# Kernel tuning notes

Measured on AMD Instinct MI355X. Metric: run time of the kernel, lower is better.

Reference implementation:

```python
import jax, jax.numpy as jnp
import numpy as np

B, T, D, HS = 8, 2048, 1024, 64  # batch, seq, num_embd, head_size


def setup_inputs() -> dict:
    key = jax.random.key(0)
    kc, kq, kk, kv = jax.random.split(key, 4)
    return {
        "context": jax.random.normal(kc, (B, T, D), dtype=jnp.float32),
        "Wq": jax.random.normal(kq, (D, HS), dtype=jnp.float32) * (D ** -0.5),
        "Wk": jax.random.normal(kk, (D, HS), dtype=jnp.float32) * (D ** -0.5),
        "Wv": jax.random.normal(kv, (D, HS), dtype=jnp.float32) * (D ** -0.5),
    }


def reference(context, Wq, Wk, Wv):
    # context: [B, T, D]; projections: [B, T, HS]
    q = context @ Wq
    k = context @ Wk
    v = context @ Wv
    scale = k.shape[-1] ** -0.5
    # scores: [B, T, T], causal mask, stable softmax (dropout p=0 -> identity)
    wei = jnp.einsum("btd,bsd->bts", q, k) * scale
    t = wei.shape[-1]
    causal = jnp.tril(jnp.ones((t, t), dtype=bool))
    wei = jnp.where(causal, wei, -jnp.inf)
    wei = jax.nn.softmax(wei, axis=-1)
    return jnp.einsum("bts,bsh->bth", wei, v)
```

## Files before the change

kernel.cpp:

```cpp
#include <hip/hip_runtime.h>
#include <math.h>

#define BB 8
#define TT 2048
#define DD 1024
#define HSZ 64

typedef __bf16 bf16_t;
typedef bf16_t bf16x8 __attribute__((ext_vector_type(8)));
typedef bf16_t bf16x4 __attribute__((ext_vector_type(4)));
typedef float f32x4 __attribute__((ext_vector_type(4)));

#define MFMA16(A, B, C) __builtin_amdgcn_mfma_f32_16x16x32_bf16(A, B, C, 0, 0, 0)


__global__ __launch_bounds__(256) void wt_convert(
    const float* __restrict__ Wq, const float* __restrict__ Wk,
    const float* __restrict__ Wv, bf16_t* __restrict__ Wtf)
{
    int id = blockIdx.x * 256 + threadIdx.x;
    int j = id & 7;
    int lane = (id >> 3) & 63;
    int chunk = (id >> 9) & 31;
    int nt = id >> 14;
    int l16 = lane & 15, quad = lane >> 4;
    int k = chunk * 32 + quad * 8 + j;
    int col = nt * 16 + l16;
    int m = col >> 6, ncol = col & 63;
    const float* W = (m == 0) ? Wq : (m == 1) ? Wk : Wv;
    float scl = (m == 0) ? 0.18033688f : 1.0f;
    Wtf[id] = (bf16_t)(W[k * HSZ + ncol] * scl);
}

__global__ __launch_bounds__(256) void qkv_proj(
    const float* __restrict__ ctx, const bf16_t* __restrict__ Wtf,
    bf16_t* __restrict__ Q, bf16_t* __restrict__ Kf, bf16_t* __restrict__ Vf)
{
    __shared__ __align__(16) char smem_raw[32 * 1032 * 2];
    bf16_t (*As)[1032] = (bf16_t (*)[1032])smem_raw;
    f32x4 (*red)[4][4][64] = (f32x4 (*)[4][4][64])smem_raw;

    const int tid = threadIdx.x;
    const int w = tid >> 6, lane = tid & 63;
    const int quad = lane >> 4, l16 = lane & 15;
    const size_t row0 = (size_t)blockIdx.x * 32;
    const int k0 = w * 256;

    {
        const float4* csrc = (const float4*)(ctx + row0 * DD);
        #pragma unroll
        for (int i = 0; i < 32; ++i) {
            float4 v = csrc[i * 256 + tid];
            bf16x4 bv;
            bv[0] = (bf16_t)v.x; bv[1] = (bf16_t)v.y;
            bv[2] = (bf16_t)v.z; bv[3] = (bf16_t)v.w;
            *(bf16x4*)&As[i][tid * 4] = bv;
        }
    }
    __syncthreads();

    f32x4 acc0[12], acc1[12];
    #pragma unroll
    for (int i = 0; i < 12; ++i) {
        acc0[i] = (f32x4){0.f, 0.f, 0.f, 0.f};
        acc1[i] = (f32x4){0.f, 0.f, 0.f, 0.f};
    }

    const bf16_t* wbase = Wtf + lane * 8;

    #pragma unroll
    for (int kc = 0; kc < 256; kc += 32) {
        const int chunk = (k0 + kc) >> 5;
        bf16x8 af0 = *(const bf16x8*)&As[l16][k0 + kc + quad * 8];
        bf16x8 af1 = *(const bf16x8*)&As[16 + l16][k0 + kc + quad * 8];
        #pragma unroll
        for (int nt = 0; nt < 12; ++nt) {
            bf16x8 bfr = *(const bf16x8*)(wbase + ((size_t)nt * 32 + chunk) * 512);
            acc0[nt] = MFMA16(af0, bfr, acc0[nt]);
            acc1[nt] = MFMA16(af1, bfr, acc1[nt]);
        }
    }
    __syncthreads();

    const int bb   = (int)(row0 >> 11);
    const int tloc = (int)(row0 & 2047);
    const int kt   = tloc >> 6;

    #pragma unroll
    for (int r = 0; r < 3; ++r) {
        if (r) __syncthreads();
        #pragma unroll
        for (int i = 0; i < 4; ++i) {
            red[0][w][i][lane] = acc0[r * 4 + i];
            red[1][w][i][lane] = acc1[r * 4 + i];
        }
        __syncthreads();

        #pragma unroll
        for (int m = 0; m < 2; ++m) {
            f32x4 s = red[m][0][w][lane];
            s += red[m][1][w][lane];
            s += red[m][2][w][lane];
            s += red[m][3][w][lane];

            const int tm = tloc + m * 16;

            if (r == 0) {
                const int col = w * 16 + l16;
                #pragma unroll
                for (int reg = 0; reg < 4; ++reg)
                    Q[(row0 + m * 16 + quad * 4 + reg) * HSZ + col] = (bf16_t)s[reg];
            } else if (r == 1) {
                const int nn = (tm >> 4) & 3;
                const int ks = w >> 1;
                const int quadf = (w & 1) * 2 + (l16 >> 3);
                const int jj = l16 & 7;
                const size_t fb = ((((size_t)bb * 32 + kt) * 4 + nn) * 2 + ks) * 512;
                #pragma unroll
                for (int reg = 0; reg < 4; ++reg)
                    Kf[fb + (quadf * 16 + quad * 4 + reg) * 8 + jj] = (bf16_t)s[reg];
            } else {
                const int t0 = tm + quad * 4;
                const int ks = (t0 >> 5) & 1;
                const int quadf = (t0 >> 3) & 3;
                const int j0 = t0 & 7;
                const size_t fb = ((((size_t)bb * 32 + kt) * 2 + ks) * 4 + w) * 512;
                bf16x4 v;
                #pragma unroll
                for (int reg = 0; reg < 4; ++reg) v[reg] = (bf16_t)s[reg];
                *(bf16x4*)(Vf + fb + (quadf * 16 + l16) * 8 + j0) = v;
            }
        }
    }
}

__device__ __forceinline__ void load_kfrags(
    const bf16_t* __restrict__ Kf, size_t bofs, int kt, int lane, bf16x8* kf)
{
    const bf16_t* kbase = Kf + ((bofs + (size_t)kt) * 8) * 512 + lane * 8;
    #pragma unroll
    for (int i = 0; i < 8; ++i)
        kf[i] = *(const bf16x8*)(kbase + i * 512);
}

__global__ __launch_bounds__(256, 3) void attn_kernel(
    const bf16_t* __restrict__ Q, const bf16_t* __restrict__ Kf,
    const bf16_t* __restrict__ Vf, float* __restrict__ O)
{
    __shared__ bf16_t Ps[4][16][72];
    __shared__ float Ored[4][16][68];
    __shared__ float Lred[4][16];

    const int tid = threadIdx.x;
    const int w = tid >> 6, lane = tid & 63;
    const int quad = lane >> 4, l16 = lane & 15;

    const int z = blockIdx.x;
    const int b = z & 7;
    const int j = 127 - (z >> 3);
    const size_t base = (size_t)b * TT * HSZ;
    const size_t bofs = (size_t)b * 32;
    const int ntile = (j >> 2) + 1, jm = j & 3;

    const bf16_t* qp = Q + base + (size_t)(j * 16 + l16) * HSZ + quad * 8;
    bf16x8 qf0 = *(const bf16x8*)qp;
    bf16x8 qf1 = *(const bf16x8*)(qp + 32);

    bf16x8 onesA;
    #pragma unroll
    for (int i = 0; i < 8; ++i) onesA[i] = (bf16_t)1.0f;

    f32x4 o[4];
    #pragma unroll
    for (int dt = 0; dt < 4; ++dt) o[dt] = (f32x4){0.f, 0.f, 0.f, 0.f};
    f32x4 lacc = (f32x4){0.f, 0.f, 0.f, 0.f};

    bf16x8 kA[8], kB[8];

    auto process = [&](int kt, const bf16x8* kf) {
        const bool last = (kt == ntile - 1);
        const int nv = last ? jm + 1 : 4;
        const int ksm = (nv > 2) ? 2 : 1;

        const bf16_t* vbase = Vf + ((bofs + (size_t)kt) * 8) * 512 + lane * 8;
        bf16x8 vf[8];
        #pragma unroll
        for (int i = 0; i < 8; ++i)
            vf[i] = *(const bf16x8*)(vbase + i * 512);

        f32x4 sc[4];
        #pragma unroll
        for (int n = 0; n < 4; ++n) {
            if (n < nv) {
                f32x4 a = (f32x4){0.f, 0.f, 0.f, 0.f};
                a = MFMA16(kf[2 * n], qf0, a);
                a = MFMA16(kf[2 * n + 1], qf1, a);
                sc[n] = a;
            }
        }

        if (last) {
            #pragma unroll
            for (int n = 0; n < 4; ++n) {
                if (n < nv) {
                    #pragma unroll
                    for (int reg = 0; reg < 4; ++reg) {
                        bool masked = (n == jm) && (quad * 4 + reg > l16);
                        float p = __builtin_amdgcn_exp2f(sc[n][reg]);
                        sc[n][reg] = masked ? 0.f : p;
                    }
                }
            }
        } else {
            #pragma unroll
            for (int n = 0; n < 4; ++n)
                #pragma unroll
                for (int reg = 0; reg < 4; ++reg)
                    sc[n][reg] = __builtin_amdgcn_exp2f(sc[n][reg]);
        }

        #pragma unroll
        for (int n = 0; n < 4; ++n) {
            bf16x4 pv;
            #pragma unroll
            for (int reg = 0; reg < 4; ++reg)
                pv[reg] = (bf16_t)((n < nv) ? sc[n][reg] : 0.f);
            *(bf16x4*)&Ps[w][l16][n * 16 + quad * 4] = pv;
        }
        bf16x8 pf0 = *(const bf16x8*)&Ps[w][l16][quad * 8];
        bf16x8 pf1 = *(const bf16x8*)&Ps[w][l16][32 + quad * 8];

        #pragma unroll
        for (int dt = 0; dt < 4; ++dt) {
            o[dt] = MFMA16(vf[dt], pf0, o[dt]);
            if (ksm == 2) o[dt] = MFMA16(vf[4 + dt], pf1, o[dt]);
        }
        lacc = MFMA16(onesA, pf0, lacc);
        if (ksm == 2) lacc = MFMA16(onesA, pf1, lacc);
    };

    if (w < ntile) {
        load_kfrags(Kf, bofs, w, lane, kA);
        for (int kt = w; kt < ntile; kt += 8) {
            if (kt + 4 < ntile) load_kfrags(Kf, bofs, kt + 4, lane, kB);
            process(kt, kA);
            if (kt + 4 < ntile) {
                if (kt + 8 < ntile) load_kfrags(Kf, bofs, kt + 8, lane, kA);
                process(kt + 4, kB);
            }
        }
    }

    #pragma unroll
    for (int dt = 0; dt < 4; ++dt)
        *(f32x4*)&Ored[w][l16][dt * 16 + quad * 4] = o[dt];
    if (quad == 0) Lred[w][l16] = lacc[0];
    __syncthreads();

    const int query = tid >> 4, d4 = tid & 15;
    float l = Lred[0][query] + Lred[1][query] + Lred[2][query] + Lred[3][query];
    f32x4 s = *(const f32x4*)&Ored[0][query][d4 * 4];
    s += *(const f32x4*)&Ored[1][query][d4 * 4];
    s += *(const f32x4*)&Ored[2][query][d4 * 4];
    s += *(const f32x4*)&Ored[3][query][d4 * 4];
    const float linv = 1.f / l;
    float4 outv = make_float4(s[0] * linv, s[1] * linv, s[2] * linv, s[3] * linv);
    *(float4*)(O + base + (size_t)(j * 16 + query) * HSZ + d4 * 4) = outv;
}

extern "C" void kernel_launch(void* const* d_in, const int* in_sizes, int n_in,
                              void* d_out, int out_size, void* d_ws, size_t ws_size,
                              hipStream_t stream) {
    const float* ctx = (const float*)d_in[0];
    const float* Wq  = (const float*)d_in[1];
    const float* Wk  = (const float*)d_in[2];
    const float* Wv  = (const float*)d_in[3];
    float* out = (float*)d_out;

    const size_t NQ = (size_t)BB * TT * HSZ;
    bf16_t* Qw  = (bf16_t*)d_ws;
    bf16_t* Kfw = Qw + NQ;
    bf16_t* Vfw = Kfw + NQ;
    bf16_t* Wtf = Vfw + NQ;

    wt_convert<<<768, 256, 0, stream>>>(Wq, Wk, Wv, Wtf);
    qkv_proj<<<512, 256, 0, stream>>>(ctx, Wtf, Qw, Kfw, Vfw);
    attn_kernel<<<1024, 256, 0, stream>>>(Qw, Kfw, Vfw, out);
}
```

Measured before the change: 123.1 us.

## Process two 16-query groups per block to reuse K/V fragments

Each attention block now handles 32 queries (two 16-row groups) instead of 16, so each K and V fragment loaded from global memory feeds twice as many MFMAs, and the grid halves to 512 blocks. Block order is reshuffled so long and short causal rows are interleaved for load balance, and the shared memory for the P staging buffer and the output reduction is aliased per wave. This costs more registers (occupancy bound lowered from 3 to 2) and gives fewer blocks to spread across CUs.

```diff
diff --git a/kernel.cpp b/kernel.cpp
--- a/kernel.cpp
+++ b/kernel.cpp
@@ -143,44 +143,56 @@
         kf[i] = *(const bf16x8*)(kbase + i * 512);
 }
 
-__global__ __launch_bounds__(256, 3) void attn_kernel(
+#define WREG 8704
+
+__global__ __launch_bounds__(256, 2) void attn_kernel(
     const bf16_t* __restrict__ Q, const bf16_t* __restrict__ Kf,
     const bf16_t* __restrict__ Vf, float* __restrict__ O)
 {
-    __shared__ bf16_t Ps[4][16][72];
-    __shared__ float Ored[4][16][68];
-    __shared__ float Lred[4][16];
+    __shared__ __align__(16) char sm[4 * WREG + 512];
 
     const int tid = threadIdx.x;
     const int w = tid >> 6, lane = tid & 63;
     const int quad = lane >> 4, l16 = lane & 15;
 
+    bf16_t (*Psw)[72] = (bf16_t (*)[72])(sm + w * WREG);
+    float  (*Orw)[68] = (float  (*)[68])(sm + w * WREG);
+    float* Lred = (float*)(sm + 4 * WREG);
+
     const int z = blockIdx.x;
     const int b = z & 7;
-    const int j = 127 - (z >> 3);
+    const int s = z >> 3;
+    const int js = (s < 32) ? (63 - s) : (s - 32);
     const size_t base = (size_t)b * TT * HSZ;
     const size_t bofs = (size_t)b * 32;
-    const int ntile = (j >> 2) + 1, jm = j & 3;
-
-    const bf16_t* qp = Q + base + (size_t)(j * 16 + l16) * HSZ + quad * 8;
-    bf16x8 qf0 = *(const bf16x8*)qp;
-    bf16x8 qf1 = *(const bf16x8*)(qp + 32);
+    const int ntile = (js >> 1) + 1;
+    const int q0 = js << 5;
+
+    bf16x8 qf0[2], qf1[2];
+    #pragma unroll
+    for (int g = 0; g < 2; ++g) {
+        const bf16_t* qp = Q + base + (size_t)(q0 + g * 16 + l16) * HSZ + quad * 8;
+        qf0[g] = *(const bf16x8*)qp;
+        qf1[g] = *(const bf16x8*)(qp + 32);
+    }
 
     bf16x8 onesA;
     #pragma unroll
     for (int i = 0; i < 8; ++i) onesA[i] = (bf16_t)1.0f;
 
-    f32x4 o[4];
-    #pragma unroll
-    for (int dt = 0; dt < 4; ++dt) o[dt] = (f32x4){0.f, 0.f, 0.f, 0.f};
-    f32x4 lacc = (f32x4){0.f, 0.f, 0.f, 0.f};
+    f32x4 o[2][4];
+    f32x4 lacc[2];
+    #pragma unroll
+    for (int g = 0; g < 2; ++g) {
+        #pragma unroll
+        for (int dt = 0; dt < 4; ++dt) o[g][dt] = (f32x4){0.f, 0.f, 0.f, 0.f};
+        lacc[g] = (f32x4){0.f, 0.f, 0.f, 0.f};
+    }
 
     bf16x8 kA[8], kB[8];
 
     auto process = [&](int kt, const bf16x8* kf) {
         const bool last = (kt == ntile - 1);
-        const int nv = last ? jm + 1 : 4;
-        const int ksm = (nv > 2) ? 2 : 1;
 
         const bf16_t* vbase = Vf + ((bofs + (size_t)kt) * 8) * 512 + lane * 8;
         bf16x8 vf[8];
@@ -188,55 +200,66 @@
         for (int i = 0; i < 8; ++i)
             vf[i] = *(const bf16x8*)(vbase + i * 512);
 
-        f32x4 sc[4];
-        #pragma unroll
-        for (int n = 0; n < 4; ++n) {
-            if (n < nv) {
-                f32x4 a = (f32x4){0.f, 0.f, 0.f, 0.f};
-                a = MFMA16(kf[2 * n], qf0, a);
-                a = MFMA16(kf[2 * n + 1], qf1, a);
-                sc[n] = a;
-            }
-        }
-
-        if (last) {
+        #pragma unroll
+        for (int g = 0; g < 2; ++g) {
+            const int jmg = (2 * js + g) & 3;
+            const int nv = last ? jmg + 1 : 4;
+
+            f32x4 sc[4];
             #pragma unroll
             for (int n = 0; n < 4; ++n) {
                 if (n < nv) {
-                    #pragma unroll
-                    for (int reg = 0; reg < 4; ++reg) {
-                        bool masked = (n == jm) && (quad * 4 + reg > l16);
-                        float p = __builtin_amdgcn_exp2f(sc[n][reg]);
-                        sc[n][reg] = masked ? 0.f : p;
+                    f32x4 a = (f32x4){0.f, 0.f, 0.f, 0.f};
+                    a = MFMA16(kf[2 * n], qf0[g], a);
+                    a = MFMA16(kf[2 * n + 1], qf1[g], a);
+                    sc[n] = a;
+                }
+            }
+
+            if (last) {
+                #pragma unroll
+                for (int n = 0; n < 4; ++n) {
+                    if (n < nv) {
+                        #pragma unroll
+                        for (int reg = 0; reg < 4; ++reg) {
+                            bool masked = (n == jmg) && (quad * 4 + reg > l16);
+                            float p = __builtin_amdgcn_exp2f(sc[n][reg]);
+                            sc[n][reg] = masked ? 0.f : p;
+                        }
                     }
                 }
-            }
-        } else {
+            } else {
+                #pragma unroll
+                for (int n = 0; n < 4; ++n)
+                    #pragma unroll
+                    for (int reg = 0; reg < 4; ++reg)
+                        sc[n][reg] = __builtin_amdgcn_exp2f(sc[n][reg]);
+            }
+
             #pragma unroll
-            for (int n = 0; n < 4; ++n)
+            for (int n = 0; n < 4; ++n) {
+                bf16x4 pv;
                 #pragma unroll
                 for (int reg = 0; reg < 4; ++reg)
-                    sc[n][reg] = __builtin_amdgcn_exp2f(sc[n][reg]);
-        }
-
-        #pragma unroll
-        for (int n = 0; n < 4; ++n) {
-            bf16x4 pv;
+                    pv[reg] = (bf16_t)((n < nv) ? sc[n][reg] : 0.f);
+                *(bf16x4*)&Psw[g * 16 + l16][n * 16 + quad * 4] = pv;
+            }
+        }
+
+        #pragma unroll
+        for (int g = 0; g < 2; ++g) {
+            const int nv = last ? ((2 * js + g) & 3) + 1 : 4;
+            const int ksm = (nv > 2) ? 2 : 1;
+            bf16x8 pf0 = *(const bf16x8*)&Psw[g * 16 + l16][quad * 8];
+            bf16x8 pf1 = *(const bf16x8*)&Psw[g * 16 + l16][32 + quad * 8];
             #pragma unroll
-            for (int reg = 0; reg < 4; ++reg)
-                pv[reg] = (bf16_t)((n < nv) ? sc[n][reg] : 0.f);
-            *(bf16x4*)&Ps[w][l16][n * 16 + quad * 4] = pv;
-        }
-        bf16x8 pf0 = *(const bf16x8*)&Ps[w][l16][quad * 8];
-        bf16x8 pf1 = *(const bf16x8*)&Ps[w][l16][32 + quad * 8];
-
-        #pragma unroll
-        for (int dt = 0; dt < 4; ++dt) {
-            o[dt] = MFMA16(vf[dt], pf0, o[dt]);
-            if (ksm == 2) o[dt] = MFMA16(vf[4 + dt], pf1, o[dt]);
-        }
-        lacc = MFMA16(onesA, pf0, lacc);
-        if (ksm == 2) lacc = MFMA16(onesA, pf1, lacc);
+            for (int dt = 0; dt < 4; ++dt) {
+                o[g][dt] = MFMA16(vf[dt], pf0, o[g][dt]);
+                if (ksm == 2) o[g][dt] = MFMA16(vf[4 + dt], pf1, o[g][dt]);
+            }
+            lacc[g] = MFMA16(onesA, pf0, lacc[g]);
+            if (ksm == 2) lacc[g] = MFMA16(onesA, pf1, lacc[g]);
+        }
     };
 
     if (w < ntile) {
@@ -252,20 +275,29 @@
     }
 
     #pragma unroll
-    for (int dt = 0; dt < 4; ++dt)
-        *(f32x4*)&Ored[w][l16][dt * 16 + quad * 4] = o[dt];
-    if (quad == 0) Lred[w][l16] = lacc[0];
+    for (int g = 0; g < 2; ++g) {
+        #pragma unroll
+        for (int dt = 0; dt < 4; ++dt)
+            *(f32x4*)&Orw[g * 16 + l16][dt * 16 + quad * 4] = o[g][dt];
+        if (quad == 0) Lred[w * 32 + g * 16 + l16] = lacc[g][0];
+    }
     __syncthreads();
 
-    const int query = tid >> 4, d4 = tid & 15;
-    float l = Lred[0][query] + Lred[1][query] + Lred[2][query] + Lred[3][query];
-    f32x4 s = *(const f32x4*)&Ored[0][query][d4 * 4];
-    s += *(const f32x4*)&Ored[1][query][d4 * 4];
-    s += *(const f32x4*)&Ored[2][query][d4 * 4];
-    s += *(const f32x4*)&Ored[3][query][d4 * 4];
-    const float linv = 1.f / l;
-    float4 outv = make_float4(s[0] * linv, s[1] * linv, s[2] * linv, s[3] * linv);
-    *(float4*)(O + base + (size_t)(j * 16 + query) * HSZ + d4 * 4) = outv;
+    #pragma unroll
+    for (int rep = 0; rep < 2; ++rep) {
+        const int idx = rep * 256 + tid;
+        const int query = idx >> 4, d4 = idx & 15;
+        float l = Lred[0 * 32 + query] + Lred[1 * 32 + query] +
+                  Lred[2 * 32 + query] + Lred[3 * 32 + query];
+        f32x4 sv = *(const f32x4*)((const float*)(sm + 0 * WREG) + query * 68 + d4 * 4);
+        sv += *(const f32x4*)((const float*)(sm + 1 * WREG) + query * 68 + d4 * 4);
+        sv += *(const f32x4*)((const float*)(sm + 2 * WREG) + query * 68 + d4 * 4);
+        sv += *(const f32x4*)((const float*)(sm + 3 * WREG) + query * 68 + d4 * 4);
+        const float linv = 1.f / l;
+        float4 outv = make_float4(sv[0] * linv, sv[1] * linv,
+                                  sv[2] * linv, sv[3] * linv);
+        *(float4*)(O + base + (size_t)(q0 + query) * HSZ + d4 * 4) = outv;
+    }
 }
 
 extern "C" void kernel_launch(void* const* d_in, const int* in_sizes, int n_in,
@@ -285,5 +317,5 @@
 
     wt_convert<<<768, 256, 0, stream>>>(Wq, Wk, Wv, Wtf);
     qkv_proj<<<512, 256, 0, stream>>>(ctx, Wtf, Qw, Kfw, Vfw);
-    attn_kernel<<<1024, 256, 0, stream>>>(Qw, Kfw, Vfw, out);
-}
+    attn_kernel<<<512, 256, 0, stream>>>(Qw, Kfw, Vfw, out);
+}
```

Result: no change. 121.7 us (-1.1%).
